# Optimization experiments

Hardware: AMD Instinct MI355X
Metric: run time of the kernel (lower is better)

## Reference

```python
import jax, jax.numpy as jnp
import numpy as np

N = 100000   # nodes
E = 1600000  # edges (avg degree 16)
Q = 64       # mesoscale velocity bins
H = 64       # collision MLP hidden dim
DT = 0.1
REG = 1e-6


def setup_inputs() -> dict:
    key = jax.random.key(0)
    ks = jax.random.split(key, 10)
    return {
        "f": jax.random.uniform(ks[0], (N, Q), jnp.float32),
        "macro_u": jax.random.normal(ks[1], (N, 1), jnp.float32),
        "source": 0.01 * jax.random.normal(ks[2], (N, Q), jnp.float32),
        "edge_src": jax.random.randint(ks[3], (E,), 0, N, jnp.int32),
        "edge_dst": jax.random.randint(ks[4], (E,), 0, N, jnp.int32),
        "edge_w": jax.random.uniform(ks[5], (E,), jnp.float32),
        "xi": jnp.linspace(-1.0, 1.0, Q).astype(jnp.float32),
        "w_in": jax.random.normal(ks[6], (Q, H), jnp.float32) / np.float32(np.sqrt(Q)),
        "b_in": jnp.zeros((H,), jnp.float32),
        "w_hid": jax.random.normal(ks[7], (3, H, H), jnp.float32) / np.float32(np.sqrt(H)),
        "b_hid": jnp.zeros((3, H), jnp.float32),
        "w_out": jax.random.normal(ks[8], (H, Q), jnp.float32) / np.float32(np.sqrt(H)),
        "b_out": jnp.zeros((Q,), jnp.float32),
    }


def _collision(f, macro_u, xi, w_in, b_in, w_hid, b_hid, w_out, b_out):
    # 5-layer MLP: relu hidden, tanh output (CollisionOperator.forward)
    x = jax.nn.relu(f @ w_in + b_in)
    for i in range(3):  # fixed small layer count, not a data-dim loop
        x = jax.nn.relu(x @ w_hid[i] + b_hid[i])
    omega = jnp.tanh(x @ w_out + b_out)                     # [N, Q]
    # Hard collision-invariance constraint: Omega* = (I - C^T (C C^T)^-1 C) Omega
    q = f.shape[1]
    w = jnp.full((q,), 1.0 / q, f.dtype)                    # quadrature weights
    xi_shifted = xi[None, :] + macro_u                      # [N, Q]
    C = jnp.stack([jnp.broadcast_to(w, xi_shifted.shape), w * xi_shifted], axis=1)  # [N,2,Q]
    CCT = jnp.einsum('naq,nbq->nab', C, C) + REG * jnp.eye(2, dtype=f.dtype)        # [N,2,2]
    v = jnp.einsum('naq,nq->na', C, omega)                  # [N,2]
    s = jnp.linalg.solve(CCT, v[..., None])[..., 0]         # [N,2]  (== CCT^-1 v)
    return omega - jnp.einsum('naq,na->nq', C, s)           # avoid dense [N,Q,Q] projection


def _transport(f, xi, edge_src, edge_dst, edge_w, n):
    # BoltzmannUpdater.compute_transport_term: both inflow (on graph) and
    # outflow (on reverse graph) reduce to the same per-edge message
    #   m_e = (w_e / out_deg[src_e]) * xi * (f[dst_e] - f[src_e])
    # aggregated at dst (inflow) and at src (outflow); transport = outflow - inflow.
    out_deg = jax.ops.segment_sum(jnp.ones_like(edge_w), edge_src, num_segments=n)
    q_e = edge_w / out_deg[edge_src]                         # [E]
    msg = q_e[:, None] * xi[None, :] * (f[edge_dst] - f[edge_src])  # [E, Q]
    inflow = jax.ops.segment_sum(msg, edge_dst, num_segments=n)
    outflow = jax.ops.segment_sum(msg, edge_src, num_segments=n)
    return outflow - inflow


def reference(f, macro_u, source, edge_src, edge_dst, edge_w, xi,
              w_in, b_in, w_hid, b_hid, w_out, b_out):
    f = jnp.maximum(f, 0.0)  # clamp(min=0)
    omega = _collision(f, macro_u, xi, w_in, b_in, w_hid, b_hid, w_out, b_out)
    trans = _transport(f, xi, edge_src, edge_dst, edge_w, f.shape[0])
    f_new = f - DT * (trans - omega - source)
    return jnp.maximum(f_new, 0.0)
```

## Files before the change

### kernel.cpp

```cpp
#include <hip/hip_runtime.h>

#define NN 100000
#define EE 1600000
#define DTc 0.1f
#define REGc 1e-6f
#define WQc (1.0f / 64.0f)

#define NB 782
#define CHUNK 2048
#define NCH 782
#define SC_NB 598
#define MPAD (SC_NB * 1024)
#define TENT (2 * EE)
#define ACT_S 72
#define PRE_NB 6250
#define WP_NB 80

typedef unsigned long long u64;
typedef __attribute__((ext_vector_type(8))) short short8;
typedef __attribute__((ext_vector_type(4))) float f32x4;

__device__ __forceinline__ unsigned short f2bf(float x) {
    unsigned u = __float_as_uint(x);
    unsigned r = (u + 0x7fffu + ((u >> 16) & 1u)) >> 16;
    return (unsigned short)r;
}
__device__ __forceinline__ float bf2f(unsigned short s) {
    return __uint_as_float(((unsigned)s) << 16);
}

__global__ __launch_bounds__(256) void prep_kernel(
    const float* __restrict__ f, unsigned int* __restrict__ fb16u,
    const float* __restrict__ w_in, const float* __restrict__ w_hid,
    const float* __restrict__ w_out, unsigned short* __restrict__ wp,
    const int* __restrict__ esrc, const int* __restrict__ edst,
    int* __restrict__ bc, int* __restrict__ deg) {
    int b = blockIdx.x;
    if (b < NCH) {
        __shared__ int cnt[NB];
        int t = threadIdx.x;
        for (int j = t; j < NB; j += 256) cnt[j] = 0;
        __syncthreads();
        int base = b * CHUNK;
        int nE = min(CHUNK, EE - base);
        int i = t * 8;
        if (i < nE) {
            int4 sa = *(const int4*)&esrc[base + i];
            int4 sb = *(const int4*)&esrc[base + i + 4];
            int4 da = *(const int4*)&edst[base + i];
            int4 db = *(const int4*)&edst[base + i + 4];
            atomicAdd(&cnt[sa.x >> 7], 1); atomicAdd(&cnt[da.x >> 7], 1); atomicAdd(&deg[sa.x], 1);
            atomicAdd(&cnt[sa.y >> 7], 1); atomicAdd(&cnt[da.y >> 7], 1); atomicAdd(&deg[sa.y], 1);
            atomicAdd(&cnt[sa.z >> 7], 1); atomicAdd(&cnt[da.z >> 7], 1); atomicAdd(&deg[sa.z], 1);
            atomicAdd(&cnt[sa.w >> 7], 1); atomicAdd(&cnt[da.w >> 7], 1); atomicAdd(&deg[sa.w], 1);
            atomicAdd(&cnt[sb.x >> 7], 1); atomicAdd(&cnt[db.x >> 7], 1); atomicAdd(&deg[sb.x], 1);
            atomicAdd(&cnt[sb.y >> 7], 1); atomicAdd(&cnt[db.y >> 7], 1); atomicAdd(&deg[sb.y], 1);
            atomicAdd(&cnt[sb.z >> 7], 1); atomicAdd(&cnt[db.z >> 7], 1); atomicAdd(&deg[sb.z], 1);
            atomicAdd(&cnt[sb.w >> 7], 1); atomicAdd(&cnt[db.w >> 7], 1); atomicAdd(&deg[sb.w], 1);
        }
        __syncthreads();
        for (int j = t; j < NB; j += 256) bc[j * NCH + b] = cnt[j];
    } else if (b < NCH + PRE_NB) {
        int i = (b - NCH) * 256 + threadIdx.x;
        float4 v = *(const float4*)&f[i * 4];
        unsigned lo = (unsigned)f2bf(fmaxf(v.x, 0.f)) | ((unsigned)f2bf(fmaxf(v.y, 0.f)) << 16);
        unsigned hi = (unsigned)f2bf(fmaxf(v.z, 0.f)) | ((unsigned)f2bf(fmaxf(v.w, 0.f)) << 16);
        fb16u[i * 2] = lo;
        fb16u[i * 2 + 1] = hi;
    } else {
        int i = (b - NCH - PRE_NB) * 256 + threadIdx.x;
        int l = i >> 12, idx = i & 4095;
        int n = idx >> 6, k = idx & 63;
        const float* W = (l == 0) ? w_in : (l < 4 ? w_hid + (l - 1) * 4096 : w_out);
        wp[i] = f2bf(W[k * 64 + n]);
    }
}

__global__ __launch_bounds__(1024) void scan_blocks(int* __restrict__ data,
                                                    int* __restrict__ bsums) {
    __shared__ int s[1024];
    int t = threadIdx.x;
    int i = blockIdx.x * 1024 + t;
    int v = data[i];
    s[t] = v;
    __syncthreads();
    for (int o = 1; o < 1024; o <<= 1) {
        int x = (t >= o) ? s[t - o] : 0;
        __syncthreads();
        s[t] += x;
        __syncthreads();
    }
    data[i] = s[t] - v;
    if (t == 0) bsums[blockIdx.x] = s[1023];
}

__global__ __launch_bounds__(1024) void scan_sums(int* __restrict__ bsums) {
    __shared__ int s[1024];
    int t = threadIdx.x;
    int v = (t < SC_NB) ? bsums[t] : 0;
    s[t] = v;
    __syncthreads();
    for (int o = 1; o < 1024; o <<= 1) {
        int x = (t >= o) ? s[t - o] : 0;
        __syncthreads();
        s[t] += x;
        __syncthreads();
    }
    if (t < SC_NB) bsums[t] = s[t] - v;
}

__device__ __forceinline__ void emit_bin(int s, int d, float w,
                                         const int* __restrict__ deg,
                                         int* cur, u64* __restrict__ adj64) {
    float q = w / (float)deg[s];
    u64 qb = ((u64)__float_as_uint(q)) << 32;
    int p1 = atomicAdd(&cur[s >> 7], 1);
    adj64[p1] = qb | (unsigned)(d | ((s & 127) << 17));
    int p2 = atomicAdd(&cur[d >> 7], 1);
    adj64[p2] = qb | (unsigned)(s | ((d & 127) << 17));
}

__global__ __launch_bounds__(256) void bin_scatter(
    const int* __restrict__ esrc, const int* __restrict__ edst,
    const float* __restrict__ ew, const int* __restrict__ deg,
    const int* __restrict__ offs, const int* __restrict__ bsums,
    u64* __restrict__ adj64) {
    __shared__ int cur[NB];
    int t = threadIdx.x, blk = blockIdx.x;
    for (int j = t; j < NB; j += 256) {
        int idx = j * NCH + blk;
        cur[j] = offs[idx] + bsums[idx >> 10];
    }
    __syncthreads();
    int base = blk * CHUNK;
    int nE = min(CHUNK, EE - base);
    int i = t * 8;
    if (i < nE) {
        int4 sa = *(const int4*)&esrc[base + i];
        int4 sb = *(const int4*)&esrc[base + i + 4];
        int4 da = *(const int4*)&edst[base + i];
        int4 db = *(const int4*)&edst[base + i + 4];
        float4 wa = *(const float4*)&ew[base + i];
        float4 wb = *(const float4*)&ew[base + i + 4];
        emit_bin(sa.x, da.x, wa.x, deg, cur, adj64);
        emit_bin(sa.y, da.y, wa.y, deg, cur, adj64);
        emit_bin(sa.z, da.z, wa.z, deg, cur, adj64);
        emit_bin(sa.w, da.w, wa.w, deg, cur, adj64);
        emit_bin(sb.x, db.x, wb.x, deg, cur, adj64);
        emit_bin(sb.y, db.y, wb.y, deg, cur, adj64);
        emit_bin(sb.z, db.z, wb.z, deg, cur, adj64);
        emit_bin(sb.w, db.w, wb.w, deg, cur, adj64);
    }
}

__global__ __launch_bounds__(256) void bucket_sort(
    const int* __restrict__ offs, const int* __restrict__ bsums,
    const u64* __restrict__ adj64,
    unsigned int* __restrict__ adj4, int* __restrict__ node_offs) {
    __shared__ int cnt[128], sc[128], base[128];
    int t = threadIdx.x, b = blockIdx.x;
    if (t < 128) cnt[t] = 0;
    __syncthreads();
    int i0 = b * NCH;
    int i1 = (b + 1) * NCH;
    int start = offs[i0] + bsums[i0 >> 10];
    int end = offs[i1] + bsums[i1 >> 10];
    for (int i = start + t; i < end; i += 256) {
        int local = ((unsigned)adj64[i] >> 17) & 127;
        atomicAdd(&cnt[local], 1);
    }
    __syncthreads();
    if (t < 128) sc[t] = cnt[t];
    __syncthreads();
    for (int o = 1; o < 128; o <<= 1) {
        int x = 0;
        if (t < 128 && t >= o) x = sc[t - o];
        __syncthreads();
        if (t < 128) sc[t] += x;
        __syncthreads();
    }
    if (t < 128) {
        base[t] = start + sc[t] - cnt[t];
        int n = b * 128 + t;
        if (n < NN) node_offs[n] = base[t];
        cnt[t] = 0;
    }
    if (b == 0 && t == 0) node_offs[NN] = TENT;
    __syncthreads();
    for (int i = start + t; i < end; i += 256) {
        u64 e = adj64[i];
        unsigned lo = (unsigned)e;
        int local = (lo >> 17) & 127;
        float q = __uint_as_float((unsigned)(e >> 32));
        unsigned q15 = (unsigned)(q * 32768.f + 0.5f);
        if (q15 > 32767u) q15 = 32767u;
        int p = base[local] + atomicAdd(&cnt[local], 1);
        adj4[p] = (q15 << 17) | (lo & 0x1FFFFu);
    }
}

#define ACC8(q, r)                                          \
    a0 = fmaf(q, __uint_as_float(r.x << 16), a0);           \
    a1 = fmaf(q, __uint_as_float(r.x & 0xFFFF0000u), a1);   \
    a2 = fmaf(q, __uint_as_float(r.y << 16), a2);           \
    a3 = fmaf(q, __uint_as_float(r.y & 0xFFFF0000u), a3);   \
    a4 = fmaf(q, __uint_as_float(r.z << 16), a4);           \
    a5 = fmaf(q, __uint_as_float(r.z & 0xFFFF0000u), a5);   \
    a6 = fmaf(q, __uint_as_float(r.w << 16), a6);           \
    a7 = fmaf(q, __uint_as_float(r.w & 0xFFFF0000u), a7);   \
    qs += q;

__global__ __launch_bounds__(256) void gather_kernel(
    const unsigned int* __restrict__ fb16u, const int* __restrict__ node_offs,
    const unsigned int* __restrict__ adj, const float* __restrict__ xi,
    float* __restrict__ trans) {
    const float QS = 1.f / 32768.f;
    int lane = threadIdx.x & 63;
    int n = blockIdx.x * 4 + (threadIdx.x >> 6);
    if (n >= NN) return;
    int c = lane & 7;
    int qt = lane >> 3;
    int j = node_offs[n];
    int end = node_offs[n + 1];
    float a0 = 0.f, a1 = 0.f, a2 = 0.f, a3 = 0.f;
    float a4 = 0.f, a5 = 0.f, a6 = 0.f, a7 = 0.f, qs = 0.f;
    for (; j + 32 <= end; j += 32) {
        unsigned e0 = __builtin_nontemporal_load(&adj[j + qt]);
        unsigned e1 = __builtin_nontemporal_load(&adj[j + 8 + qt]);
        unsigned e2 = __builtin_nontemporal_load(&adj[j + 16 + qt]);
        unsigned e3 = __builtin_nontemporal_load(&adj[j + 24 + qt]);
        uint4 r0 = *(const uint4*)&fb16u[(e0 & 0x1FFFFu) * 32 + c * 4];
        uint4 r1 = *(const uint4*)&fb16u[(e1 & 0x1FFFFu) * 32 + c * 4];
        uint4 r2 = *(const uint4*)&fb16u[(e2 & 0x1FFFFu) * 32 + c * 4];
        uint4 r3 = *(const uint4*)&fb16u[(e3 & 0x1FFFFu) * 32 + c * 4];
        float q0 = (float)(e0 >> 17) * QS;
        float q1 = (float)(e1 >> 17) * QS;
        float q2 = (float)(e2 >> 17) * QS;
        float q3 = (float)(e3 >> 17) * QS;
        ACC8(q0, r0)
        ACC8(q1, r1)
        ACC8(q2, r2)
        ACC8(q3, r3)
    }
    for (; j + 8 <= end; j += 8) {
        unsigned e = __builtin_nontemporal_load(&adj[j + qt]);
        uint4 r = *(const uint4*)&fb16u[(e & 0x1FFFFu) * 32 + c * 4];
        float q = (float)(e >> 17) * QS;
        ACC8(q, r)
    }
    if (j < end) {
        int idx = j + qt;
        bool ok = idx < end;
        unsigned e = ok ? adj[idx] : 0u;
        uint4 r = *(const uint4*)&fb16u[(e & 0x1FFFFu) * 32 + c * 4];
        float q = ok ? (float)(e >> 17) * QS : 0.f;
        ACC8(q, r)
    }
#define RED3(x) x += __shfl_xor(x, 8); x += __shfl_xor(x, 16); x += __shfl_xor(x, 32)
    RED3(a0); RED3(a1); RED3(a2); RED3(a3);
    RED3(a4); RED3(a5); RED3(a6); RED3(a7); RED3(qs);
    if (qt == 0) {
        uint4 rn = *(const uint4*)&fb16u[n * 32 + c * 4];
        float4 x0 = *(const float4*)&xi[c * 8];
        float4 x1 = *(const float4*)&xi[c * 8 + 4];
        f32x4 o0, o1;
        o0.x = x0.x * (a0 - qs * __uint_as_float(rn.x << 16));
        o0.y = x0.y * (a1 - qs * __uint_as_float(rn.x & 0xFFFF0000u));
        o0.z = x0.z * (a2 - qs * __uint_as_float(rn.y << 16));
        o0.w = x0.w * (a3 - qs * __uint_as_float(rn.y & 0xFFFF0000u));
        o1.x = x1.x * (a4 - qs * __uint_as_float(rn.z << 16));
        o1.y = x1.y * (a5 - qs * __uint_as_float(rn.z & 0xFFFF0000u));
        o1.z = x1.z * (a6 - qs * __uint_as_float(rn.w << 16));
        o1.w = x1.w * (a7 - qs * __uint_as_float(rn.w & 0xFFFF0000u));
        __builtin_nontemporal_store(o0, (f32x4*)&trans[n * 64 + c * 8]);
        __builtin_nontemporal_store(o1, (f32x4*)&trans[n * 64 + c * 8 + 4]);
    }
}

__global__ __launch_bounds__(256) void node_kernel(
    const unsigned short* __restrict__ fb16, const float* __restrict__ f,
    const float* __restrict__ macro_u, const float* __restrict__ source,
    const float* __restrict__ xi, const unsigned short* __restrict__ wp,
    const float* __restrict__ b_in, const float* __restrict__ b_hid,
    const float* __restrict__ b_out,
    const float* __restrict__ trans, float* __restrict__ out) {
    __shared__ __attribute__((aligned(16))) unsigned short act[128 * ACT_S];
    __shared__ float s0s[128], s1s[128], us[128], xif[64];

    const int t = threadIdx.x;
    const int wid = t >> 6;
    const int lane = t & 63;
    const int m = lane & 15;
    const int quad = lane >> 4;
    const int nodeBase = blockIdx.x * 128;
    const int gbase = nodeBase * 64;

    if (t < 128) {
        int n = nodeBase + t;
        us[t] = (n < NN) ? macro_u[n] : 0.f;
    }
    if (t < 64) xif[t] = xi[t];

#pragma unroll
    for (int i = 0; i < 8; i++) {
        int r = wid * 32 + i * 4 + (lane >> 4);
        int c = (lane & 15) * 4;
        uint2 v = {0u, 0u};
        if (nodeBase + r < NN) v = *(const uint2*)&fb16[gbase + r * 64 + c];
        *(uint2*)&act[r * ACT_S + c] = v;
    }

    const int rowbase = wid * 32;

    for (int l = 0; l < 5; l++) {
        const unsigned short* W = wp + l * 4096;
        const float* B = (l == 0) ? b_in : (l < 4 ? b_hid + (l - 1) * 64 : b_out);

        short8 Af[2][2], Bf[4][2];
#pragma unroll
        for (int rt = 0; rt < 2; rt++)
#pragma unroll
            for (int kk = 0; kk < 2; kk++)
                Af[rt][kk] = *(const short8*)&act[(rowbase + rt * 16 + m) * ACT_S + kk * 32 + quad * 8];
#pragma unroll
        for (int ct = 0; ct < 4; ct++)
#pragma unroll
            for (int kk = 0; kk < 2; kk++)
                Bf[ct][kk] = *(const short8*)&W[(ct * 16 + m) * 64 + kk * 32 + quad * 8];

        f32x4 acc[2][4];
#pragma unroll
        for (int rt = 0; rt < 2; rt++)
#pragma unroll
            for (int ct = 0; ct < 4; ct++) {
                acc[rt][ct] = (f32x4){0.f, 0.f, 0.f, 0.f};
                acc[rt][ct] = __builtin_amdgcn_mfma_f32_16x16x32_bf16(Af[rt][0], Bf[ct][0], acc[rt][ct], 0, 0, 0);
                acc[rt][ct] = __builtin_amdgcn_mfma_f32_16x16x32_bf16(Af[rt][1], Bf[ct][1], acc[rt][ct], 0, 0, 0);
            }

#pragma unroll
        for (int rt = 0; rt < 2; rt++)
#pragma unroll
            for (int ct = 0; ct < 4; ct++) {
                float bv = B[ct * 16 + m];
#pragma unroll
                for (int r = 0; r < 4; r++) {
                    int row = rowbase + rt * 16 + quad * 4 + r;
                    float val = acc[rt][ct][r] + bv;
                    val = (l < 4) ? fmaxf(val, 0.f) : tanhf(val);
                    act[row * ACT_S + ct * 16 + m] = f2bf(val);
                }
            }
    }
    __syncthreads();

    if (t < 128) {
        float u = us[t];
        float v0 = 0.f, v1 = 0.f, sxs2 = 0.f, sxi = 0.f;
        const short8* rp = (const short8*)&act[t * ACT_S];
#pragma unroll
        for (int c = 0; c < 8; c++) {
            short8 v = rp[c];
#pragma unroll
            for (int jj = 0; jj < 8; jj++) {
                float om = bf2f((unsigned short)v[jj]);
                float xv = xif[c * 8 + jj];
                float xs = xv + u;
                v0 += om;
                v1 += xs * om;
                sxs2 += xs * xs;
                sxi += xv;
            }
        }
        v0 *= WQc;
        v1 *= WQc;
        float c00 = WQc + REGc;
        float c01 = WQc * WQc * (sxi + 64.f * u);
        float c11 = WQc * WQc * sxs2 + REGc;
        float det = c00 * c11 - c01 * c01;
        float inv = 1.0f / det;
        s0s[t] = (c11 * v0 - c01 * v1) * inv;
        s1s[t] = (c00 * v1 - c01 * v0) * inv;
    }
    __syncthreads();

#pragma unroll
    for (int i = 0; i < 8; i++) {
        int e = (i * 256 + t) * 4;
        int nl = e >> 6;
        if (nodeBase + nl < NN) {
            int g = gbase + e;
            int c0 = e & 63;
            float4 fv = *(const float4*)&f[g];
            float4 sv = *(const float4*)&source[g];
            float4 tv = *(const float4*)&trans[g];
            float uu = us[nl];
            float sv0 = s0s[nl], sv1 = s1s[nl];
            float4 ov;
            float* ovp = (float*)&ov;
            const float* fp = (const float*)&fv;
            const float* sp = (const float*)&sv;
            const float* tp = (const float*)&tv;
#pragma unroll
            for (int jj = 0; jj < 4; jj++) {
                float om = bf2f(act[nl * ACT_S + c0 + jj]);
                float xs = xif[c0 + jj] + uu;
                float omst = om - WQc * (sv0 + xs * sv1);
                float val = fmaxf(fp[jj], 0.f) + DTc * (sp[jj] + omst - tp[jj]);
                ovp[jj] = fmaxf(val, 0.f);
            }
            *(float4*)&out[g] = ov;
        }
    }
}

extern "C" void kernel_launch(void* const* d_in, const int* in_sizes, int n_in,
                              void* d_out, int out_size, void* d_ws, size_t ws_size,
                              hipStream_t stream) {
    const float* f       = (const float*)d_in[0];
    const float* macro_u = (const float*)d_in[1];
    const float* source  = (const float*)d_in[2];
    const int*   esrc    = (const int*)d_in[3];
    const int*   edst    = (const int*)d_in[4];
    const float* ew      = (const float*)d_in[5];
    const float* xi      = (const float*)d_in[6];
    const float* w_in    = (const float*)d_in[7];
    const float* b_in    = (const float*)d_in[8];
    const float* w_hid   = (const float*)d_in[9];
    const float* b_hid   = (const float*)d_in[10];
    const float* w_out   = (const float*)d_in[11];
    const float* b_out   = (const float*)d_in[12];
    float* out = (float*)d_out;

    u64* adj64 = (u64*)d_ws;
    unsigned int* adj4 = (unsigned int*)(adj64 + TENT);
    int* deg   = (int*)(adj4 + TENT);
    int* bc    = deg + NN;
    int* bsums = bc + MPAD;
    int* node_offs = bsums + 1024;
    float* trans = (float*)(node_offs + NN + 8);
    unsigned short* fb16 = (unsigned short*)(trans + (size_t)NN * 64);
    unsigned short* wp = fb16 + (size_t)NN * 64;

    hipMemsetAsync(deg, 0, (size_t)(NN + MPAD) * sizeof(int), stream);

    prep_kernel<<<NCH + PRE_NB + WP_NB, 256, 0, stream>>>(
        f, (unsigned int*)fb16, w_in, w_hid, w_out, wp, esrc, edst, bc, deg);
    scan_blocks<<<SC_NB, 1024, 0, stream>>>(bc, bsums);
    scan_sums<<<1, 1024, 0, stream>>>(bsums);
    bin_scatter<<<NCH, 256, 0, stream>>>(esrc, edst, ew, deg, bc, bsums, adj64);
    bucket_sort<<<NB, 256, 0, stream>>>(bc, bsums, adj64, adj4, node_offs);
    gather_kernel<<<(NN + 3) / 4, 256, 0, stream>>>((const unsigned int*)fb16,
                                                    node_offs, adj4, xi, trans);
    node_kernel<<<(NN + 127) / 128, 256, 0, stream>>>(
        fb16, f, macro_u, source, xi, wp, b_in, b_hid, b_out, trans, out);
}
```

Baseline: 398.0 us.

## Derive out-degree from bucket histogram instead of global atomics

Removes the 1.6M global atomicAdds on deg in prep_kernel and the random deg[s] lookup in bin_scatter. Source-side entries are tagged with a side bit, so the per-bucket histogram pass can count out-degree in shared memory. The bucket sort is split into a histogram kernel and a scatter kernel, and the scatter kernel divides the weight by degree at that point. The cost is an extra kernel launch and a random deg[other] read for destination-side entries in the scatter.

```diff
diff --git a/kernel.cpp b/kernel.cpp
--- a/kernel.cpp
+++ b/kernel.cpp
@@ -15,6 +15,7 @@
 #define ACT_S 72
 #define PRE_NB 6250
 #define WP_NB 80
+#define SIDE_BIT (1u << 24)
 
 typedef unsigned long long u64;
 typedef __attribute__((ext_vector_type(8))) short short8;
@@ -34,7 +35,7 @@
     const float* __restrict__ w_in, const float* __restrict__ w_hid,
     const float* __restrict__ w_out, unsigned short* __restrict__ wp,
     const int* __restrict__ esrc, const int* __restrict__ edst,
-    int* __restrict__ bc, int* __restrict__ deg) {
+    int* __restrict__ bc) {
     int b = blockIdx.x;
     if (b < NCH) {
         __shared__ int cnt[NB];
@@ -49,14 +50,14 @@
             int4 sb = *(const int4*)&esrc[base + i + 4];
             int4 da = *(const int4*)&edst[base + i];
             int4 db = *(const int4*)&edst[base + i + 4];
-            atomicAdd(&cnt[sa.x >> 7], 1); atomicAdd(&cnt[da.x >> 7], 1); atomicAdd(&deg[sa.x], 1);
-            atomicAdd(&cnt[sa.y >> 7], 1); atomicAdd(&cnt[da.y >> 7], 1); atomicAdd(&deg[sa.y], 1);
-            atomicAdd(&cnt[sa.z >> 7], 1); atomicAdd(&cnt[da.z >> 7], 1); atomicAdd(&deg[sa.z], 1);
-            atomicAdd(&cnt[sa.w >> 7], 1); atomicAdd(&cnt[da.w >> 7], 1); atomicAdd(&deg[sa.w], 1);
-            atomicAdd(&cnt[sb.x >> 7], 1); atomicAdd(&cnt[db.x >> 7], 1); atomicAdd(&deg[sb.x], 1);
-            atomicAdd(&cnt[sb.y >> 7], 1); atomicAdd(&cnt[db.y >> 7], 1); atomicAdd(&deg[sb.y], 1);
-            atomicAdd(&cnt[sb.z >> 7], 1); atomicAdd(&cnt[db.z >> 7], 1); atomicAdd(&deg[sb.z], 1);
-            atomicAdd(&cnt[sb.w >> 7], 1); atomicAdd(&cnt[db.w >> 7], 1); atomicAdd(&deg[sb.w], 1);
+            atomicAdd(&cnt[sa.x >> 7], 1); atomicAdd(&cnt[da.x >> 7], 1);
+            atomicAdd(&cnt[sa.y >> 7], 1); atomicAdd(&cnt[da.y >> 7], 1);
+            atomicAdd(&cnt[sa.z >> 7], 1); atomicAdd(&cnt[da.z >> 7], 1);
+            atomicAdd(&cnt[sa.w >> 7], 1); atomicAdd(&cnt[da.w >> 7], 1);
+            atomicAdd(&cnt[sb.x >> 7], 1); atomicAdd(&cnt[db.x >> 7], 1);
+            atomicAdd(&cnt[sb.y >> 7], 1); atomicAdd(&cnt[db.y >> 7], 1);
+            atomicAdd(&cnt[sb.z >> 7], 1); atomicAdd(&cnt[db.z >> 7], 1);
+            atomicAdd(&cnt[sb.w >> 7], 1); atomicAdd(&cnt[db.w >> 7], 1);
         }
         __syncthreads();
         for (int j = t; j < NB; j += 256) bc[j * NCH + b] = cnt[j];
@@ -109,20 +110,9 @@
     if (t < SC_NB) bsums[t] = s[t] - v;
 }
 
-__device__ __forceinline__ void emit_bin(int s, int d, float w,
-                                         const int* __restrict__ deg,
-                                         int* cur, u64* __restrict__ adj64) {
-    float q = w / (float)deg[s];
-    u64 qb = ((u64)__float_as_uint(q)) << 32;
-    int p1 = atomicAdd(&cur[s >> 7], 1);
-    adj64[p1] = qb | (unsigned)(d | ((s & 127) << 17));
-    int p2 = atomicAdd(&cur[d >> 7], 1);
-    adj64[p2] = qb | (unsigned)(s | ((d & 127) << 17));
-}
-
 __global__ __launch_bounds__(256) void bin_scatter(
     const int* __restrict__ esrc, const int* __restrict__ edst,
-    const float* __restrict__ ew, const int* __restrict__ deg,
+    const float* __restrict__ ew,
     const int* __restrict__ offs, const int* __restrict__ bsums,
     u64* __restrict__ adj64) {
     __shared__ int cur[NB];
@@ -142,35 +132,42 @@
         int4 db = *(const int4*)&edst[base + i + 4];
         float4 wa = *(const float4*)&ew[base + i];
         float4 wb = *(const float4*)&ew[base + i + 4];
-        emit_bin(sa.x, da.x, wa.x, deg, cur, adj64);
-        emit_bin(sa.y, da.y, wa.y, deg, cur, adj64);
-        emit_bin(sa.z, da.z, wa.z, deg, cur, adj64);
-        emit_bin(sa.w, da.w, wa.w, deg, cur, adj64);
-        emit_bin(sb.x, db.x, wb.x, deg, cur, adj64);
-        emit_bin(sb.y, db.y, wb.y, deg, cur, adj64);
-        emit_bin(sb.z, db.z, wb.z, deg, cur, adj64);
-        emit_bin(sb.w, db.w, wb.w, deg, cur, adj64);
-    }
-}
-
-__global__ __launch_bounds__(256) void bucket_sort(
+#define EMIT(s, d, w)                                                         \
+        {                                                                     \
+            u64 wb64 = ((u64)__float_as_uint(w)) << 32;                       \
+            int p1 = atomicAdd(&cur[(s) >> 7], 1);                            \
+            adj64[p1] = wb64 | SIDE_BIT | (unsigned)((d) | (((s) & 127) << 17)); \
+            int p2 = atomicAdd(&cur[(d) >> 7], 1);                            \
+            adj64[p2] = wb64 | (unsigned)((s) | (((d) & 127) << 17));         \
+        }
+        EMIT(sa.x, da.x, wa.x) EMIT(sa.y, da.y, wa.y)
+        EMIT(sa.z, da.z, wa.z) EMIT(sa.w, da.w, wa.w)
+        EMIT(sb.x, db.x, wb.x) EMIT(sb.y, db.y, wb.y)
+        EMIT(sb.z, db.z, wb.z) EMIT(sb.w, db.w, wb.w)
+#undef EMIT
+    }
+}
+
+__global__ __launch_bounds__(256) void bucket_histo(
     const int* __restrict__ offs, const int* __restrict__ bsums,
     const u64* __restrict__ adj64,
-    unsigned int* __restrict__ adj4, int* __restrict__ node_offs) {
-    __shared__ int cnt[128], sc[128], base[128];
+    int* __restrict__ node_offs, int* __restrict__ deg) {
+    __shared__ int cnt_tot[128], cnt_src[128], sc[128];
     int t = threadIdx.x, b = blockIdx.x;
-    if (t < 128) cnt[t] = 0;
+    if (t < 128) { cnt_tot[t] = 0; cnt_src[t] = 0; }
     __syncthreads();
     int i0 = b * NCH;
     int i1 = (b + 1) * NCH;
     int start = offs[i0] + bsums[i0 >> 10];
     int end = offs[i1] + bsums[i1 >> 10];
     for (int i = start + t; i < end; i += 256) {
-        int local = ((unsigned)adj64[i] >> 17) & 127;
-        atomicAdd(&cnt[local], 1);
-    }
-    __syncthreads();
-    if (t < 128) sc[t] = cnt[t];
+        unsigned lo = (unsigned)adj64[i];
+        int local = (lo >> 17) & 127;
+        atomicAdd(&cnt_tot[local], 1);
+        if (lo & SIDE_BIT) atomicAdd(&cnt_src[local], 1);
+    }
+    __syncthreads();
+    if (t < 128) sc[t] = cnt_tot[t];
     __syncthreads();
     for (int o = 1; o < 128; o <<= 1) {
         int x = 0;
@@ -180,22 +177,44 @@
         __syncthreads();
     }
     if (t < 128) {
-        base[t] = start + sc[t] - cnt[t];
         int n = b * 128 + t;
-        if (n < NN) node_offs[n] = base[t];
-        cnt[t] = 0;
+        if (n < NN) {
+            node_offs[n] = start + sc[t] - cnt_tot[t];
+            deg[n] = cnt_src[t];
+        }
     }
     if (b == 0 && t == 0) node_offs[NN] = TENT;
-    __syncthreads();
+}
+
+__global__ __launch_bounds__(256) void bucket_scatter(
+    const int* __restrict__ offs, const int* __restrict__ bsums,
+    const u64* __restrict__ adj64, const int* __restrict__ node_offs,
+    const int* __restrict__ deg, unsigned int* __restrict__ adj4) {
+    __shared__ int cur[128];
+    __shared__ float ldeg[128];
+    int t = threadIdx.x, b = blockIdx.x;
+    if (t < 128) {
+        int n = b * 128 + t;
+        cur[t] = (n < NN) ? node_offs[n] : 0;
+        ldeg[t] = (n < NN) ? (float)deg[n] : 1.f;
+    }
+    __syncthreads();
+    int i0 = b * NCH;
+    int i1 = (b + 1) * NCH;
+    int start = offs[i0] + bsums[i0 >> 10];
+    int end = offs[i1] + bsums[i1 >> 10];
     for (int i = start + t; i < end; i += 256) {
         u64 e = adj64[i];
         unsigned lo = (unsigned)e;
         int local = (lo >> 17) & 127;
-        float q = __uint_as_float((unsigned)(e >> 32));
+        unsigned other = lo & 0x1FFFFu;
+        float w = __uint_as_float((unsigned)(e >> 32));
+        float dv = (lo & SIDE_BIT) ? ldeg[local] : (float)deg[other];
+        float q = w / dv;
         unsigned q15 = (unsigned)(q * 32768.f + 0.5f);
         if (q15 > 32767u) q15 = 32767u;
-        int p = base[local] + atomicAdd(&cnt[local], 1);
-        adj4[p] = (q15 << 17) | (lo & 0x1FFFFu);
+        int p = atomicAdd(&cur[local], 1);
+        adj4[p] = (q15 << 17) | other;
     }
 }
 
@@ -442,14 +461,15 @@
     unsigned short* fb16 = (unsigned short*)(trans + (size_t)NN * 64);
     unsigned short* wp = fb16 + (size_t)NN * 64;
 
-    hipMemsetAsync(deg, 0, (size_t)(NN + MPAD) * sizeof(int), stream);
+    hipMemsetAsync(bc, 0, (size_t)MPAD * sizeof(int), stream);
 
     prep_kernel<<<NCH + PRE_NB + WP_NB, 256, 0, stream>>>(
-        f, (unsigned int*)fb16, w_in, w_hid, w_out, wp, esrc, edst, bc, deg);
+        f, (unsigned int*)fb16, w_in, w_hid, w_out, wp, esrc, edst, bc);
     scan_blocks<<<SC_NB, 1024, 0, stream>>>(bc, bsums);
     scan_sums<<<1, 1024, 0, stream>>>(bsums);
-    bin_scatter<<<NCH, 256, 0, stream>>>(esrc, edst, ew, deg, bc, bsums, adj64);
-    bucket_sort<<<NB, 256, 0, stream>>>(bc, bsums, adj64, adj4, node_offs);
+    bin_scatter<<<NCH, 256, 0, stream>>>(esrc, edst, ew, bc, bsums, adj64);
+    bucket_histo<<<NB, 256, 0, stream>>>(bc, bsums, adj64, node_offs, deg);
+    bucket_scatter<<<NB, 256, 0, stream>>>(bc, bsums, adj64, node_offs, deg, adj4);
     gather_kernel<<<(NN + 3) / 4, 256, 0, stream>>>((const unsigned int*)fb16,
                                                     node_offs, adj4, xi, trans);
     node_kernel<<<(NN + 127) / 128, 256, 0, stream>>>(
```

Result: faster. 336.4 us (-15.5%).
